# Optimization experiments

Hardware: AMD Instinct MI355X
Metric: run time of the kernel (lower is better)

Reference implementation:

```python
import jax, jax.numpy as jnp
import numpy as np

B, T, D = 4, 2048, 1024
H = 16
HD = D // H  # 64


def setup_inputs() -> dict:
    key = jax.random.key(0)
    ks = jax.random.split(key, 7)
    scale = 1.0 / np.sqrt(D)
    x = jax.random.normal(ks[0], (B, T, D), dtype=jnp.float32)
    # per-head projection weights, stacked over heads: [H, D, HD]
    Wq = jax.random.normal(ks[1], (H, D, HD), dtype=jnp.float32) * scale
    Wk = jax.random.normal(ks[2], (H, D, HD), dtype=jnp.float32) * scale
    Wv = jax.random.normal(ks[3], (H, D, HD), dtype=jnp.float32) * scale
    s_raw = jnp.zeros((H,), dtype=jnp.float32)  # learnable ssmax scale per head
    proj_W = jax.random.normal(ks[4], (D, D), dtype=jnp.float32) * scale
    proj_b = jax.random.normal(ks[5], (D,), dtype=jnp.float32) * 0.01
    return {"x": x, "Wq": Wq, "Wk": Wk, "Wv": Wv, "s_raw": s_raw,
            "proj_W": proj_W, "proj_b": proj_b}


def reference(x, Wq, Wk, Wv, s_raw, proj_W, proj_b):
    # per-head q/k/v: [B, H, T, HD]
    q = jnp.einsum('btd,hde->bhte', x, Wq)
    k = jnp.einsum('btd,hde->bhte', x, Wk)
    v = jnp.einsum('btd,hde->bhte', x, Wv)

    # ssmax: q scaled by softplus(s) * log(position index, 1-based)
    logn = jnp.log(jnp.arange(1, T + 1, dtype=x.dtype))  # [T]
    s = jax.nn.softplus(s_raw)  # [H]
    q = q * (s[None, :, None, None] * logn[None, None, :, None])

    scores = jnp.einsum('bhte,bhse->bhts', q, k) * (HD ** -0.5)
    causal = jnp.tril(jnp.ones((T, T), dtype=bool))
    scores = jnp.where(causal[None, None], scores, -jnp.inf)
    w = jax.nn.softmax(scores, axis=-1)

    out = jnp.einsum('bhts,bhse->bhte', w, v)          # [B, H, T, HD]
    out = out.transpose(0, 2, 1, 3).reshape(B, T, D)    # concat heads
    return out @ proj_W.T + proj_b
```

## Files before the change

kernel.cpp:

```cpp
#include <hip/hip_runtime.h>
#include <hip/hip_bf16.h>

#define Bv 4
#define Tv 2048
#define Dv 1024
#define Hv 16
#define HDv 64
#define Mv (Bv*Tv)

typedef __hip_bfloat16 bf16;
typedef short s8v __attribute__((ext_vector_type(8)));
typedef float f4v __attribute__((ext_vector_type(4)));
typedef float f16a __attribute__((ext_vector_type(16)));

__device__ __forceinline__ unsigned short f2us(float x){
    bf16 h = __float2bfloat16(x);
    return *reinterpret_cast<unsigned short*>(&h);
}
__device__ __forceinline__ unsigned int pack2(float a, float b){
    return (unsigned int)f2us(a) | ((unsigned int)f2us(b) << 16);
}
__device__ __forceinline__ void glds16(const unsigned short* g, unsigned short* lds_base){
    __builtin_amdgcn_global_load_lds(
        (const __attribute__((address_space(1))) unsigned int*)g,
        (__attribute__((address_space(3))) unsigned int*)lds_base, 16, 0, 0);
}

__global__ void cvt_kernel(const float* __restrict__ src,
                           unsigned short* __restrict__ dst, int n4) {
    int i = blockIdx.x * 256 + threadIdx.x;
    if (i < n4) {
        float4 f = *(const float4*)(src + (size_t)i * 4);
        ushort4 o;
        o.x = f2us(f.x); o.y = f2us(f.y); o.z = f2us(f.z); o.w = f2us(f.w);
        *(ushort4*)(dst + (size_t)i * 4) = o;
    }
}

__global__ __launch_bounds__(256) void wt_kernel(
    const float* __restrict__ Wq, const float* __restrict__ Wk,
    const float* __restrict__ Wv, unsigned short* __restrict__ Wt)
{
    const int dt  = blockIdx.x;
    const int h   = blockIdx.y;
    const int sel = blockIdx.z;
    const float* W = (sel == 0) ? Wq : ((sel == 1) ? Wk : Wv);
    const float* Wh = W + (size_t)h * Dv * HDv;
    __shared__ float Tf[64][65];
    const int tid = threadIdx.x;
    for (int l = 0; l < 16; ++l) {
        int idx = tid + l * 256;
        int r = idx >> 6, e = idx & 63;
        Tf[r][e] = Wh[(size_t)(dt * 64 + r) * HDv + e];
    }
    __syncthreads();
    unsigned short* out = Wt + ((size_t)sel * Hv + h) * HDv * Dv;
    for (int l = 0; l < 16; ++l) {
        int idx = tid + l * 256;
        int e = idx >> 6, d = idx & 63;
        out[(size_t)e * Dv + dt * 64 + d] = f2us(Tf[d][e]);
    }
}

__global__ __launch_bounds__(512, 2) void qkv_8ph(
    const unsigned short* __restrict__ xb, const unsigned short* __restrict__ Wc,
    const float* __restrict__ s_raw,
    unsigned short* __restrict__ q, unsigned short* __restrict__ k,
    unsigned short* __restrict__ vT)
{
    extern __shared__ unsigned short smem[];
    const int lid  = blockIdx.x;
    const int xcd  = lid & 7;
    const int slot = lid >> 3;
    const int bm   = xcd * 4 + (slot & 3);
    const int bn   = slot >> 2;
    const int tid = threadIdx.x;
    const int w = tid >> 6, lane = tid & 63;
    const int wm = w >> 2, wn = w & 3;
    const int n16 = lane & 15, quad = lane >> 4, l7 = lane & 7;

    const int row0 = bm * 256, col0 = bn * 256;

    const int sr = lane >> 3;
    const int sc = ((lane & 7) ^ (sr & 7)) * 8;

    f4v acc[8][4];
    f4v zero = {0.f, 0.f, 0.f, 0.f};
    #pragma unroll
    for (int i = 0; i < 8; ++i)
        #pragma unroll
        for (int j = 0; j < 4; ++j) acc[i][j] = zero;

    s8v Ar[8][2];
    s8v Br[4][2];

    auto stageA = [&](int b, int h, int tk){
        const unsigned short* g = xb + ((size_t)(row0 + h*128 + w*16 + sr)) * Dv + tk*64 + sc;
        unsigned short* l = smem + b*32768 + h*8192 + w*1024;
        glds16(g, l);
        glds16(g + 8*Dv, l + 512);
    };
    auto stageB = [&](int b, int h, int tk){
        const unsigned short* g = Wc + ((size_t)(col0 + h*128 + w*16 + sr)) * Dv + tk*64 + sc;
        unsigned short* l = smem + b*32768 + 16384 + h*8192 + w*1024;
        glds16(g, l);
        glds16(g + 8*Dv, l + 512);
    };
    auto readA = [&](int b, int mh){
        #pragma unroll
        for (int mi = 0; mi < 4; ++mi)
            #pragma unroll
            for (int kk = 0; kk < 2; ++kk)
                Ar[mh*4+mi][kk] = *(const s8v*)(smem + b*32768 + wm*8192
                    + ((mh*4+mi)*16 + n16) * 64 + (((kk*4 + quad) ^ l7) * 8));
    };
    auto readB = [&](int b, int nh){
        #pragma unroll
        for (int ni = 0; ni < 2; ++ni)
            #pragma unroll
            for (int kk = 0; kk < 2; ++kk)
                Br[nh*2+ni][kk] = *(const s8v*)(smem + b*32768 + 16384 + (wn>>1)*8192
                    + ((wn&1)*64 + (nh*2+ni)*16 + n16) * 64 + (((kk*4 + quad) ^ l7) * 8));
    };
    auto quadMM = [&](int mh, int nh){
        #pragma unroll
        for (int kk = 0; kk < 2; ++kk)
            #pragma unroll
            for (int mi = 0; mi < 4; ++mi)
                #pragma unroll
                for (int ni = 0; ni < 2; ++ni)
                    acc[mh*4+mi][nh*2+ni] = __builtin_amdgcn_mfma_f32_16x16x32_bf16(
                        Ar[mh*4+mi][kk], Br[nh*2+ni][kk], acc[mh*4+mi][nh*2+ni], 0, 0, 0);
    };

    stageA(0,0,0); stageA(0,1,0); stageB(0,0,0); stageB(0,1,0);
    stageA(1,0,1); stageA(1,1,1); stageB(1,0,1); stageB(1,1,1);
    asm volatile("s_waitcnt vmcnt(8)" ::: "memory");
    __builtin_amdgcn_s_barrier();

    #pragma unroll 1
    for (int it = 0; it < 8; ++it) {
        const bool nl = (it < 7);
        const int t2 = 2*it + 2, t3 = 2*it + 3;
        readA(0,0); readB(0,0);
        __builtin_amdgcn_s_barrier();
        __builtin_amdgcn_s_setprio(1); quadMM(0,0); __builtin_amdgcn_s_setprio(0);
        __builtin_amdgcn_s_barrier();
        readA(0,1);
        __builtin_amdgcn_s_barrier();
        __builtin_amdgcn_s_setprio(1); quadMM(1,0); __builtin_amdgcn_s_setprio(0);
        __builtin_amdgcn_s_barrier();
        readB(0,1);
        if (nl) stageA(0,0,t2);
        __builtin_amdgcn_s_barrier();
        __builtin_amdgcn_s_setprio(1); quadMM(1,1); __builtin_amdgcn_s_setprio(0);
        asm volatile("s_waitcnt lgkmcnt(0)" ::: "memory");
        __builtin_amdgcn_s_barrier();
        if (nl) stageA(0,1,t2);
        __builtin_amdgcn_s_barrier();
        __builtin_amdgcn_s_setprio(1); quadMM(0,1); __builtin_amdgcn_s_setprio(0);
        if (nl) { asm volatile("s_waitcnt vmcnt(4)" ::: "memory"); }
        else    { asm volatile("s_waitcnt vmcnt(0)" ::: "memory"); }
        __builtin_amdgcn_s_barrier();
        readA(1,0); readB(1,0);
        if (nl) stageB(0,0,t2);
        __builtin_amdgcn_s_barrier();
        __builtin_amdgcn_s_setprio(1); quadMM(0,0); __builtin_amdgcn_s_setprio(0);
        __builtin_amdgcn_s_barrier();
        readA(1,1);
        if (nl) stageB(0,1,t2);
        __builtin_amdgcn_s_barrier();
        __builtin_amdgcn_s_setprio(1); quadMM(1,0); __builtin_amdgcn_s_setprio(0);
        __builtin_amdgcn_s_barrier();
        readB(1,1);
        if (nl) { stageA(1,0,t3); stageA(1,1,t3); }
        __builtin_amdgcn_s_barrier();
        __builtin_amdgcn_s_setprio(1); quadMM(1,1); __builtin_amdgcn_s_setprio(0);
        asm volatile("s_waitcnt lgkmcnt(0)" ::: "memory");
        __builtin_amdgcn_s_barrier();
        if (nl) { stageB(1,0,t3); stageB(1,1,t3); }
        __builtin_amdgcn_s_barrier();
        __builtin_amdgcn_s_setprio(1); quadMM(0,1); __builtin_amdgcn_s_setprio(0);
        if (nl) { asm volatile("s_waitcnt vmcnt(8)" ::: "memory"); }
        __builtin_amdgcn_s_barrier();
    }

    const int sel = bn >> 2;
    const int h = (bn * 4 + wn) & 15;
    if (sel == 2) {
        #pragma unroll
        for (int ni = 0; ni < 4; ++ni) {
            int e = ni * 16 + n16;
            #pragma unroll
            for (int mi = 0; mi < 8; ++mi) {
                int row = row0 + wm * 128 + mi * 16 + quad * 4;
                int bb_ = row >> 11, t = row & (Tv - 1);
                ushort4 o4;
                o4.x = f2us(acc[mi][ni][0]); o4.y = f2us(acc[mi][ni][1]);
                o4.z = f2us(acc[mi][ni][2]); o4.w = f2us(acc[mi][ni][3]);
                *(ushort4*)(vT + ((size_t)(bb_ * Hv + h) * HDv + e) * Tv + t) = o4;
            }
        }
    } else {
        unsigned short* outp = (sel == 0) ? q : k;
        const float sc_h = (sel == 0) ? log1pf(expf(s_raw[h])) * 0.125f : 1.0f;
        unsigned short* ep = smem + w * 8192;
        const int colq = (bn & 3) * 256 + wn * 64;
        #pragma unroll
        for (int mi = 0; mi < 8; ++mi) {
            #pragma unroll
            for (int r = 0; r < 4; ++r) {
                const int lrow = mi * 16 + quad * 4 + r;
                const int t = (row0 + wm * 128 + lrow) & (Tv - 1);
                const float rs = (sel == 0) ? sc_h * __logf((float)(t + 1)) : 1.0f;
                #pragma unroll
                for (int ni = 0; ni < 4; ++ni)
                    ep[lrow * 64 + ((ni * 16 + n16) ^ (quad * 16))] = f2us(acc[mi][ni][r] * rs);
            }
        }
        #pragma unroll
        for (int i = 0; i < 16; ++i) {
            const int rrow = i * 8 + (lane >> 3);
            const int key = ((rrow >> 2) & 3) * 16;
            s8v vv = *(const s8v*)(ep + rrow * 64 + (((lane & 7) * 8) ^ key));
            *(s8v*)(outp + (size_t)(row0 + wm * 128 + rrow) * Dv + colq + (lane & 7) * 8) = vv;
        }
    }
}

__global__ __launch_bounds__(256) void attn_mfma(
    const unsigned short* __restrict__ q, const unsigned short* __restrict__ k,
    const unsigned short* __restrict__ vT, unsigned short* __restrict__ attn)
{
    const int bh = blockIdx.y;
    const int b = bh >> 4, h = bh & 15;
    const int tid = threadIdx.x;
    const int w = tid >> 6, lane = tid & 63;
    const int l31 = lane & 31, hi = lane >> 5;

    __shared__ __align__(16) unsigned short Ks[128][72];
    __shared__ __align__(16) unsigned short VTs[64][136];

    const size_t qkbase = (size_t)b * Tv * Dv + h * HDv;
    const unsigned short* kb = k + qkbase;
    const unsigned short* vb = vT + (size_t)(b * Hv + h) * Tv * HDv;

    for (int phase = 0; phase < 2; ++phase) {
        const int qt = phase ? (15 - (int)blockIdx.x) : (int)blockIdx.x;
        const int qstrip = qt * 128 + w * 32;
        const int myq = qstrip + l31;

        s8v qf[4];
        #pragma unroll
        for (int ks = 0; ks < 4; ++ks)
            qf[ks] = *(const s8v*)(q + qkbase + (size_t)myq * Dv + ks * 16 + hi * 8);

        f16a st[4], ot0, ot1;
        #pragma unroll
        for (int i = 0; i < 16; ++i) { ot0[i] = 0.f; ot1[i] = 0.f; }
        float lrun = 0.f;

        for (int ss = 0; ss <= qt; ++ss) {
            const int s0 = ss * 128;
            __syncthreads();
            #pragma unroll
            for (int l = 0; l < 4; ++l) {
                int idx = tid + l * 256;
                int r = idx >> 3, c = (idx & 7) * 8;
                *(ulonglong2*)(&Ks[r][c]) =
                    *(const ulonglong2*)(kb + (size_t)(s0 + r) * Dv + c);
            }
            #pragma unroll
            for (int l = 0; l < 4; ++l) {
                int idx = tid + l * 256;
                int e = idx >> 4, c = (idx & 15) * 8;
                *(ulonglong2*)(&VTs[e][c]) =
                    *(const ulonglong2*)(vb + (size_t)e * Tv + s0 + c);
            }
            __syncthreads();

            #pragma unroll
            for (int mt = 0; mt < 4; ++mt)
                #pragma unroll
                for (int i = 0; i < 16; ++i) st[mt][i] = 0.f;
            #pragma unroll
            for (int ks = 0; ks < 4; ++ks) {
                #pragma unroll
                for (int mt = 0; mt < 4; ++mt) {
                    s8v a = *(const s8v*)(&Ks[32 * mt + l31][ks * 16 + hi * 8]);
                    st[mt] = __builtin_amdgcn_mfma_f32_32x32x16_bf16(a, qf[ks], st[mt], 0, 0, 0);
                }
            }
            if (s0 + 127 > qstrip) {
                #pragma unroll
                for (int mt = 0; mt < 4; ++mt)
                    #pragma unroll
                    for (int reg = 0; reg < 16; ++reg) {
                        int srow = (reg & 3) + 8 * (reg >> 2) + 4 * hi;
                        if (s0 + 32 * mt + srow > myq) st[mt][reg] = -1e30f;
                    }
            }
            float lsum = 0.f;
            #pragma unroll
            for (int mt = 0; mt < 4; ++mt)
                #pragma unroll
                for (int i = 0; i < 16; ++i) {
                    st[mt][i] = __expf(st[mt][i]);
                    lsum += st[mt][i];
                }
            lrun += lsum;

            #pragma unroll
            for (int half = 0; half < 2; ++half) {
                unsigned int pk[16];
                #pragma unroll
                for (int g = 0; g < 4; ++g) {
                    pk[2*g]       = pack2(st[2*half][4*g],     st[2*half][4*g+1]);
                    pk[2*g+1]     = pack2(st[2*half][4*g+2],   st[2*half][4*g+3]);
                    pk[8+2*g]     = pack2(st[2*half+1][4*g],   st[2*half+1][4*g+1]);
                    pk[8+2*g+1]   = pack2(st[2*half+1][4*g+2], st[2*half+1][4*g+3]);
                }
                #pragma unroll
                for (int ks4 = 0; ks4 < 4; ++ks4) {
                    const int ks = half * 4 + ks4;
                    const int base = (ks4 >> 1) * 8 + (ks4 & 1) * 4;
                    unsigned int v0 = hi ? pk[base]     : pk[base + 2];
                    unsigned int v1 = hi ? pk[base + 1] : pk[base + 3];
                    unsigned int r0 = (unsigned int)__shfl_xor((int)v0, 32);
                    unsigned int r1 = (unsigned int)__shfl_xor((int)v1, 32);
                    union { s8v v; unsigned int d[4]; } bf;
                    bf.d[0] = hi ? r0 : pk[base];
                    bf.d[1] = hi ? r1 : pk[base + 1];
                    bf.d[2] = hi ? pk[base + 2] : r0;
                    bf.d[3] = hi ? pk[base + 3] : r1;
                    s8v a0 = *(const s8v*)(&VTs[l31][ks * 16 + hi * 8]);
                    s8v a1 = *(const s8v*)(&VTs[32 + l31][ks * 16 + hi * 8]);
                    ot0 = __builtin_amdgcn_mfma_f32_32x32x16_bf16(a0, bf.v, ot0, 0, 0, 0);
                    ot1 = __builtin_amdgcn_mfma_f32_32x32x16_bf16(a1, bf.v, ot1, 0, 0, 0);
                }
            }
        }

        float ltot = lrun + __shfl_xor(lrun, 32);
        float inv = 1.0f / ltot;
        size_t obase = ((size_t)(b * Tv) + myq) * Dv + h * HDv;
        #pragma unroll
        for (int g = 0; g < 4; ++g) {
            ushort4 o4;
            o4.x = f2us(ot0[4*g]   * inv); o4.y = f2us(ot0[4*g+1] * inv);
            o4.z = f2us(ot0[4*g+2] * inv); o4.w = f2us(ot0[4*g+3] * inv);
            *(ushort4*)(attn + obase + 8 * g + 4 * hi) = o4;
            o4.x = f2us(ot1[4*g]   * inv); o4.y = f2us(ot1[4*g+1] * inv);
            o4.z = f2us(ot1[4*g+2] * inv); o4.w = f2us(ot1[4*g+3] * inv);
            *(ushort4*)(attn + obase + 32 + 8 * g + 4 * hi) = o4;
        }
    }
}

__global__ __launch_bounds__(256) void proj_big(
    const unsigned short* __restrict__ attn, const unsigned short* __restrict__ Wb,
    const float* __restrict__ bias, float* __restrict__ out)
{
    const int bm = blockIdx.x;
    const int bn = blockIdx.y;
    const int tid = threadIdx.x;
    const int w = tid >> 6, lane = tid & 63;
    const int n16 = lane & 15, quad = lane >> 4;
    const int wm = w >> 1, wn = w & 1;

    __shared__ __align__(16) unsigned short As[128 * 64];
    __shared__ __align__(16) unsigned short Bs[128 * 64];

    f4v acc[4][4];
    f4v zero = {0.f, 0.f, 0.f, 0.f};
    #pragma unroll
    for (int i = 0; i < 4; ++i)
        #pragma unroll
        for (int j = 0; j < 4; ++j) acc[i][j] = zero;

    const int row0 = bm * 128, col0 = bn * 128;
    const int lr = lane >> 3, lc = (lane & 7) * 8;

    for (int k0 = 0; k0 < Dv; k0 += 64) {
        __syncthreads();
        #pragma unroll
        for (int i = 0; i < 4; ++i) {
            int rb = w * 32 + i * 8;
            glds16(attn + (size_t)(row0 + rb + lr) * Dv + k0 + lc, &As[rb * 64]);
            glds16(Wb   + (size_t)(col0 + rb + lr) * Dv + k0 + lc, &Bs[rb * 64]);
        }
        __syncthreads();
        #pragma unroll
        for (int ks = 0; ks < 2; ++ks) {
            s8v bfr[4];
            #pragma unroll
            for (int ni = 0; ni < 4; ++ni)
                bfr[ni] = *(const s8v*)(&Bs[(wn * 64 + ni * 16 + n16) * 64 + ks * 32 + quad * 8]);
            #pragma unroll
            for (int mi = 0; mi < 4; ++mi) {
                s8v afr = *(const s8v*)(&As[(wm * 64 + mi * 16 + n16) * 64 + ks * 32 + quad * 8]);
                #pragma unroll
                for (int ni = 0; ni < 4; ++ni)
                    acc[mi][ni] = __builtin_amdgcn_mfma_f32_16x16x32_bf16(afr, bfr[ni], acc[mi][ni], 0, 0, 0);
            }
        }
    }
    #pragma unroll
    for (int ni = 0; ni < 4; ++ni) {
        int n = col0 + wn * 64 + ni * 16 + n16;
        float bn_ = bias[n];
        #pragma unroll
        for (int mi = 0; mi < 4; ++mi) {
            #pragma unroll
            for (int r = 0; r < 4; ++r) {
                int m = row0 + wm * 64 + mi * 16 + quad * 4 + r;
                out[(size_t)m * Dv + n] = acc[mi][ni][r] + bn_;
            }
        }
    }
}

extern "C" void kernel_launch(void* const* d_in, const int* in_sizes, int n_in,
                              void* d_out, int out_size, void* d_ws, size_t ws_size,
                              hipStream_t stream) {
    const float* x     = (const float*)d_in[0];
    const float* Wq    = (const float*)d_in[1];
    const float* Wk    = (const float*)d_in[2];
    const float* Wv    = (const float*)d_in[3];
    const float* s_raw = (const float*)d_in[4];
    const float* projW = (const float*)d_in[5];
    const float* projb = (const float*)d_in[6];
    float* out = (float*)d_out;

    const size_t nx  = (size_t)Mv * Dv;
    const size_t nqk = (size_t)Bv * Hv * Tv * HDv;
    unsigned short* x_bf = (unsigned short*)d_ws;
    unsigned short* qb   = x_bf + nx;
    unsigned short* kb   = qb + nqk;
    unsigned short* vTb  = kb + nqk;
    unsigned short* Wt   = vTb + nqk;
    unsigned short* Wpb  = Wt + (size_t)3 * Hv * HDv * Dv;
    unsigned short* attn = x_bf;

    static int cfg = 0;
    if (!cfg) {
        (void)hipFuncSetAttribute((const void*)qkv_8ph,
                                  hipFuncAttributeMaxDynamicSharedMemorySize, 131072);
        cfg = 1;
    }

    cvt_kernel<<<(int)(nx / 4 / 256), 256, 0, stream>>>(x, x_bf, (int)(nx / 4));
    cvt_kernel<<<(int)((size_t)Dv * Dv / 4 / 256), 256, 0, stream>>>(projW, Wpb, Dv * Dv / 4);
    wt_kernel<<<dim3(16, 16, 3), 256, 0, stream>>>(Wq, Wk, Wv, Wt);
    qkv_8ph<<<dim3(384), 512, 131072, stream>>>(x_bf, Wt, s_raw, qb, kb, vTb);
    attn_mfma<<<dim3(8, Bv * Hv), 256, 0, stream>>>(qb, kb, vTb, attn);
    proj_big<<<dim3(Mv / 128, Dv / 128), 256, 0, stream>>>(attn, Wpb, projb, out);
}
```

Measured before the change: 266.1 us.

## Reorder QKV GEMM mainloop quadrant schedule and peel final iteration

Restructures the ping-pong MFMA mainloop of the QKV projection GEMM. Quadrants are now computed in a different order (0,0 / 0,1 / 1,0 / 1,1), with register reads and global-to-LDS staging interleaved at new points. The last iteration is peeled into a barrier-light epilogue, which removes the per-iteration 'nl' branches. The intent is better overlap of LDS reads, global loads and MFMA work with fewer barriers in the tail, at the risk of new LDS hazards or register-reuse timing issues.

```diff
diff --git a/kernel.cpp b/kernel.cpp
--- a/kernel.cpp
+++ b/kernel.cpp
@@ -139,51 +139,58 @@
     __builtin_amdgcn_s_barrier();
 
     #pragma unroll 1
-    for (int it = 0; it < 8; ++it) {
-        const bool nl = (it < 7);
+    for (int it = 0; it < 7; ++it) {
         const int t2 = 2*it + 2, t3 = 2*it + 3;
         readA(0,0); readB(0,0);
         __builtin_amdgcn_s_barrier();
         __builtin_amdgcn_s_setprio(1); quadMM(0,0); __builtin_amdgcn_s_setprio(0);
         __builtin_amdgcn_s_barrier();
-        readA(0,1);
+        readB(0,1); readA(0,1);
+        __builtin_amdgcn_s_barrier();
+        __builtin_amdgcn_s_setprio(1); quadMM(0,1); __builtin_amdgcn_s_setprio(0);
+        asm volatile("s_waitcnt lgkmcnt(0)" ::: "memory");
+        __builtin_amdgcn_s_barrier();
+        stageA(0,0,t2);
         __builtin_amdgcn_s_barrier();
         __builtin_amdgcn_s_setprio(1); quadMM(1,0); __builtin_amdgcn_s_setprio(0);
         __builtin_amdgcn_s_barrier();
-        readB(0,1);
-        if (nl) stageA(0,0,t2);
+        stageA(0,1,t2);
         __builtin_amdgcn_s_barrier();
         __builtin_amdgcn_s_setprio(1); quadMM(1,1); __builtin_amdgcn_s_setprio(0);
+        asm volatile("s_waitcnt vmcnt(4)" ::: "memory");
+        __builtin_amdgcn_s_barrier();
+        readA(1,0); readB(1,0); stageB(0,0,t2);
+        __builtin_amdgcn_s_barrier();
+        __builtin_amdgcn_s_setprio(1); quadMM(0,0); __builtin_amdgcn_s_setprio(0);
+        __builtin_amdgcn_s_barrier();
+        readB(1,1); readA(1,1); stageB(0,1,t2);
+        __builtin_amdgcn_s_barrier();
+        __builtin_amdgcn_s_setprio(1); quadMM(0,1); __builtin_amdgcn_s_setprio(0);
         asm volatile("s_waitcnt lgkmcnt(0)" ::: "memory");
         __builtin_amdgcn_s_barrier();
-        if (nl) stageA(0,1,t2);
-        __builtin_amdgcn_s_barrier();
-        __builtin_amdgcn_s_setprio(1); quadMM(0,1); __builtin_amdgcn_s_setprio(0);
-        if (nl) { asm volatile("s_waitcnt vmcnt(4)" ::: "memory"); }
-        else    { asm volatile("s_waitcnt vmcnt(0)" ::: "memory"); }
-        __builtin_amdgcn_s_barrier();
-        readA(1,0); readB(1,0);
-        if (nl) stageB(0,0,t2);
-        __builtin_amdgcn_s_barrier();
-        __builtin_amdgcn_s_setprio(1); quadMM(0,0); __builtin_amdgcn_s_setprio(0);
-        __builtin_amdgcn_s_barrier();
-        readA(1,1);
-        if (nl) stageB(0,1,t2);
+        stageA(1,0,t3); stageA(1,1,t3);
         __builtin_amdgcn_s_barrier();
         __builtin_amdgcn_s_setprio(1); quadMM(1,0); __builtin_amdgcn_s_setprio(0);
         __builtin_amdgcn_s_barrier();
-        readB(1,1);
-        if (nl) { stageA(1,0,t3); stageA(1,1,t3); }
+        stageB(1,0,t3); stageB(1,1,t3);
         __builtin_amdgcn_s_barrier();
         __builtin_amdgcn_s_setprio(1); quadMM(1,1); __builtin_amdgcn_s_setprio(0);
-        asm volatile("s_waitcnt lgkmcnt(0)" ::: "memory");
-        __builtin_amdgcn_s_barrier();
-        if (nl) { stageB(1,0,t3); stageB(1,1,t3); }
-        __builtin_amdgcn_s_barrier();
-        __builtin_amdgcn_s_setprio(1); quadMM(0,1); __builtin_amdgcn_s_setprio(0);
-        if (nl) { asm volatile("s_waitcnt vmcnt(8)" ::: "memory"); }
-        __builtin_amdgcn_s_barrier();
-    }
+        asm volatile("s_waitcnt vmcnt(8)" ::: "memory");
+        __builtin_amdgcn_s_barrier();
+    }
+
+    readA(0,0); readB(0,0); readB(0,1); readA(0,1);
+    __builtin_amdgcn_s_setprio(1);
+    quadMM(0,0); quadMM(0,1); quadMM(1,0); quadMM(1,1);
+    __builtin_amdgcn_s_setprio(0);
+    asm volatile("s_waitcnt vmcnt(0)" ::: "memory");
+    __builtin_amdgcn_s_barrier();
+    readA(1,0); readB(1,0); readB(1,1); readA(1,1);
+    __builtin_amdgcn_s_setprio(1);
+    quadMM(0,0); quadMM(0,1); quadMM(1,0); quadMM(1,1);
+    __builtin_amdgcn_s_setprio(0);
+    asm volatile("s_waitcnt lgkmcnt(0)" ::: "memory");
+    __builtin_amdgcn_s_barrier();
 
     const int sel = bn >> 2;
     const int h = (bn * 4 + wn) & 15;
```

Result: slower. 319.7 us (+20.1%).
